# Kernel optimization log

Hardware: AMD Instinct MI355X
Metric: run time of the kernel (lower is better)

The kernel has to match this reference:

```python
import jax, jax.numpy as jnp
import numpy as np

FILTERS = 256
KH, KW = 3, 3
SH, SW = 1, 1
IN_CH = 128


def setup_inputs() -> dict:
    key = jax.random.key(0)
    k1, k2 = jax.random.split(key)
    inputs = jax.random.normal(k1, (32, 112, 112, IN_CH), dtype=jnp.float32)
    # Glorot-uniform init matching the layer's build()
    limit = np.sqrt(6.0 / (KH * KW * IN_CH + FILTERS)).astype(np.float32)
    kernel = jax.random.uniform(k2, (KH, KW, IN_CH, FILTERS), dtype=jnp.float32,
                                minval=-limit, maxval=limit)
    bias = jnp.zeros((FILTERS,), dtype=jnp.float32)
    return {"inputs": inputs, "kernel": kernel, "bias": bias}


def reference(inputs, kernel, bias):
    # Equivalent math to extract_patches(SAME) + flattened matmul + bias:
    # a standard 2D convolution in NHWC with HWIO kernel.
    out = jax.lax.conv_general_dilated(
        inputs, kernel,
        window_strides=(SH, SW),
        padding="SAME",
        dimension_numbers=("NHWC", "HWIO", "NHWC"),
    )
    return out + bias
```

## Files before the change

### kernel.cpp

```cpp
#include <hip/hip_runtime.h>

typedef __attribute__((ext_vector_type(4))) float   floatx4;
typedef __attribute__((ext_vector_type(8))) __bf16  bf16x8;
typedef unsigned short ushort_t;
typedef __attribute__((ext_vector_type(8))) ushort_t ushortx8;

typedef const unsigned int __attribute__((address_space(1)))* gptr_t;
typedef unsigned int __attribute__((address_space(3)))* lptr_t;

#define NIMG 32
#define H    112
#define W    112
#define CIN  128
#define COUT 256
#define HP   114
#define WP   114
#define HW   12544

#define BM 256
#define BN 256
#define BK 64
#define NT 18

#define PREPAD_BLOCKS 12996
#define WTRANS_BLOCKS 1152

__device__ __forceinline__ ushort_t f32_to_bf16(float f) {
    unsigned u = __float_as_uint(f);
    unsigned r = 0x7fffu + ((u >> 16) & 1u);
    return (ushort_t)((u + r) >> 16);
}

__global__ __launch_bounds__(256) void prepass_fused(const float* __restrict__ in,
                                                     const float* __restrict__ k,
                                                     ushort_t* __restrict__ pad,
                                                     ushort_t* __restrict__ wt) {
    int bid = blockIdx.x;
    if (bid < PREPAD_BLOCKS) {
        int u    = bid * 256 + threadIdx.x;
        int ic16 = u & 7;
        int sp   = u >> 3;
        int iw   = sp % WP;
        int sp2  = sp / WP;
        int ih   = sp2 % HP;
        int n    = sp2 / HP;
        ushortx8 v0, v1;
        if (ih >= 1 && ih <= H && iw >= 1 && iw <= W) {
            const float* src = in + ((size_t)((n * H + (ih - 1)) * W + (iw - 1))) * CIN + ic16 * 16;
            floatx4 a = *reinterpret_cast<const floatx4*>(src);
            floatx4 b = *reinterpret_cast<const floatx4*>(src + 4);
            floatx4 c = *reinterpret_cast<const floatx4*>(src + 8);
            floatx4 d = *reinterpret_cast<const floatx4*>(src + 12);
#pragma unroll
            for (int j = 0; j < 4; ++j) {
                v0[j] = f32_to_bf16(a[j]); v0[4 + j] = f32_to_bf16(b[j]);
                v1[j] = f32_to_bf16(c[j]); v1[4 + j] = f32_to_bf16(d[j]);
            }
        } else {
#pragma unroll
            for (int j = 0; j < 8; ++j) { v0[j] = 0; v1[j] = 0; }
        }
        ushortx8* dst = reinterpret_cast<ushortx8*>(pad) + ((size_t)sp * 16 + ic16 * 2);
        dst[0] = v0;
        dst[1] = v1;
    } else {
        int t    = (bid - PREPAD_BLOCKS) * 256 + threadIdx.x;
        int ic   = t & 127;
        int oc   = (t >> 7) & 255;
        int khkw = t >> 15;
        wt[t] = f32_to_bf16(k[((size_t)(khkw * CIN + ic)) * COUT + oc]);
    }
}


__device__ __forceinline__ int aoffK(int t) {
    int tap = t >> 1;
    return ((tap / 3) * WP + (tap % 3)) * CIN + (t & 1) * 64;
}
__device__ __forceinline__ int boffK(int t) {
    int tap = t >> 1;
    return tap * (COUT * CIN) + (t & 1) * 64;
}

__global__ __launch_bounds__(512, 2) void conv_mfma8(const ushort_t* __restrict__ pad,
                                                     const ushort_t* __restrict__ wt,
                                                     const float* __restrict__ bias,
                                                     float* __restrict__ out) {
    __shared__ __align__(16) ushort_t lds[65536];

    const int tid  = threadIdx.x;
    const int wid  = tid >> 6;
    const int lane = tid & 63;
    const int wm   = wid >> 2;
    const int wn   = wid & 3;
    const int bid  = blockIdx.x;
    const int bm   = (bid & 7) * 196 + (bid >> 3);

    const int trow = tid >> 3;
    const int lc   = (tid & 7) ^ (trow & 7);

    const ushort_t* srcA[4];
    const ushort_t* srcB[4];
#pragma unroll
    for (int i = 0; i < 4; ++i) {
        int m  = bm * BM + i * 64 + trow;
        int n  = m / HW;
        int r  = m % HW;
        int oh = r / W;
        int ow = r % W;
        srcA[i] = pad + ((size_t)((n * HP + oh) * WP + ow)) * CIN + lc * 8;
        int oc = i * 64 + trow;
        srcB[i] = wt + (size_t)oc * CIN + lc * 8;
    }
    const int dstSlot = wid * 512;

#define STAGE_A(tile, half)                                                                         \
    { int _o = aoffK(tile); int _b = ((tile) & 1) * 32768 + (half) * 8192 + dstSlot;                \
      __builtin_amdgcn_global_load_lds((gptr_t)(srcA[(half)*2+0] + _o), (lptr_t)&lds[_b       ], 16, 0, 0); \
      __builtin_amdgcn_global_load_lds((gptr_t)(srcA[(half)*2+1] + _o), (lptr_t)&lds[_b + 4096], 16, 0, 0); }
#define STAGE_B(tile, half)                                                                         \
    { int _o = boffK(tile); int _b = ((tile) & 1) * 32768 + 16384 + (half) * 8192 + dstSlot;        \
      __builtin_amdgcn_global_load_lds((gptr_t)(srcB[(half)*2+0] + _o), (lptr_t)&lds[_b       ], 16, 0, 0); \
      __builtin_amdgcn_global_load_lds((gptr_t)(srcB[(half)*2+1] + _o), (lptr_t)&lds[_b + 4096], 16, 0, 0); }

    const int aBase = wm * 8192 + (lane & 15) * 64;
    const int bBase = 16384 + (wn >> 1) * 8192 + ((wn & 1) * 64 + (lane & 15)) * 64;
    int cOff[2];
#pragma unroll
    for (int ks = 0; ks < 2; ++ks)
        cOff[ks] = ((ks * 4 + (lane >> 4)) ^ (lane & 7)) * 8;

    floatx4 acc[8][4];
#pragma unroll
    for (int i = 0; i < 8; ++i)
#pragma unroll
        for (int j = 0; j < 4; ++j) acc[i][j] = (floatx4)0.0f;

    STAGE_A(0, 0); STAGE_A(0, 1); STAGE_B(0, 0); STAGE_B(0, 1);
    STAGE_B(1, 0); STAGE_B(1, 1);
    asm volatile("s_waitcnt vmcnt(4)" ::: "memory");
    __builtin_amdgcn_s_barrier();

    for (int t = 0; t < NT; ++t) {
        const int bufb = (t & 1) * 32768;
        bf16x8 bfr[4][2];
#pragma unroll
        for (int q = 0; q < 4; ++q) {
            bf16x8 af[2][2];
#pragma unroll
            for (int rfl = 0; rfl < 2; ++rfl)
#pragma unroll
                for (int ks = 0; ks < 2; ++ks)
                    af[rfl][ks] = *reinterpret_cast<const bf16x8*>(&lds[bufb + aBase + (2 * q + rfl) * 1024 + cOff[ks]]);
            if (q == 0) {
#pragma unroll
                for (int cf = 0; cf < 2; ++cf)
#pragma unroll
                    for (int ks = 0; ks < 2; ++ks)
                        bfr[cf][ks] = *reinterpret_cast<const bf16x8*>(&lds[bufb + bBase + cf * 1024 + cOff[ks]]);
            }
            if (q == 0 && t + 1 < NT) STAGE_A(t + 1, 0);
            if (q == 1 && t + 1 < NT) STAGE_A(t + 1, 1);
            if (q == 2 && t + 2 < NT) STAGE_B(t + 2, 0);
            if (q == 3 && t + 2 < NT) STAGE_B(t + 2, 1);
            __builtin_amdgcn_s_barrier();
            __builtin_amdgcn_s_setprio(1);
            if (q == 0) {
#pragma unroll
                for (int rfl = 0; rfl < 2; ++rfl)
#pragma unroll
                    for (int cf = 0; cf < 2; ++cf)
#pragma unroll
                        for (int ks = 0; ks < 2; ++ks)
                            acc[rfl][cf] = __builtin_amdgcn_mfma_f32_16x16x32_bf16(
                                af[rfl][ks], bfr[cf][ks], acc[rfl][cf], 0, 0, 0);
#pragma unroll
                for (int cf = 2; cf < 4; ++cf)
#pragma unroll
                    for (int ks = 0; ks < 2; ++ks)
                        bfr[cf][ks] = *reinterpret_cast<const bf16x8*>(&lds[bufb + bBase + cf * 1024 + cOff[ks]]);
#pragma unroll
                for (int rfl = 0; rfl < 2; ++rfl)
#pragma unroll
                    for (int cf = 2; cf < 4; ++cf)
#pragma unroll
                        for (int ks = 0; ks < 2; ++ks)
                            acc[rfl][cf] = __builtin_amdgcn_mfma_f32_16x16x32_bf16(
                                af[rfl][ks], bfr[cf][ks], acc[rfl][cf], 0, 0, 0);
            } else {
#pragma unroll
                for (int rfl = 0; rfl < 2; ++rfl)
#pragma unroll
                    for (int cf = 0; cf < 4; ++cf)
#pragma unroll
                        for (int ks = 0; ks < 2; ++ks)
                            acc[2 * q + rfl][cf] = __builtin_amdgcn_mfma_f32_16x16x32_bf16(
                                af[rfl][ks], bfr[cf][ks], acc[2 * q + rfl][cf], 0, 0, 0);
            }
            __builtin_amdgcn_s_setprio(0);
            if (q == 3) {
                if (t < NT - 2)       { asm volatile("s_waitcnt vmcnt(4)" ::: "memory"); }
                else if (t == NT - 2) { asm volatile("s_waitcnt vmcnt(0)" ::: "memory"); }
            }
            __builtin_amdgcn_s_barrier();
        }
    }

    const int col0 = wn * 64 + (lane & 15);
    const int row0 = bm * BM + wm * 128 + (lane >> 4) * 4;
    float bv[4];
#pragma unroll
    for (int cf = 0; cf < 4; ++cf) bv[cf] = bias[col0 + cf * 16];
#pragma unroll
    for (int rf = 0; rf < 8; ++rf)
#pragma unroll
        for (int cf = 0; cf < 4; ++cf)
#pragma unroll
            for (int r = 0; r < 4; ++r)
                out[(size_t)(row0 + rf * 16 + r) * COUT + col0 + cf * 16] = acc[rf][cf][r] + bv[cf];
#undef STAGE_A
#undef STAGE_B
}

extern "C" void kernel_launch(void* const* d_in, const int* in_sizes, int n_in,
                              void* d_out, int out_size, void* d_ws, size_t ws_size,
                              hipStream_t stream) {
    const float* input = (const float*)d_in[0];
    const float* kern  = (const float*)d_in[1];
    const float* bias  = (const float*)d_in[2];
    float* out         = (float*)d_out;

    ushort_t* pad = (ushort_t*)d_ws;
    ushort_t* wt  = pad + (size_t)NIMG * HP * WP * CIN;

    prepass_fused<<<PREPAD_BLOCKS + WTRANS_BLOCKS, 256, 0, stream>>>(input, kern, pad, wt);
    conv_mfma8<<<1568, 512, 0, stream>>>(pad, wt, bias, out);
}
```

Before: 358.6 us.

## Replace LDS double buffer with single buffer and fine-grained chunk refills

Halves the conv kernel's shared memory from 128KB to 64KB by dropping the double buffer. Each 32-row A chunk and each B half is refilled as soon as the quarter-step that reads it has finished, with per-quarter vmcnt waits. The likely aim is lower LDS footprint, which could let more blocks fit per CU, while keeping loads overlapped with MFMA work. The cost is shorter prefetch distance and tighter waits, so load latency may be exposed more often, and the hand-counted vmcnt values must match exactly to avoid races.

```diff
diff --git a/kernel.cpp b/kernel.cpp
--- a/kernel.cpp
+++ b/kernel.cpp
@@ -72,7 +72,6 @@
     }
 }
 
-
 __device__ __forceinline__ int aoffK(int t) {
     int tap = t >> 1;
     return ((tap / 3) * WP + (tap % 3)) * CIN + (t & 1) * 64;
@@ -81,12 +80,13 @@
     int tap = t >> 1;
     return tap * (COUT * CIN) + (t & 1) * 64;
 }
+
 
 __global__ __launch_bounds__(512, 2) void conv_mfma8(const ushort_t* __restrict__ pad,
                                                      const ushort_t* __restrict__ wt,
                                                      const float* __restrict__ bias,
                                                      float* __restrict__ out) {
-    __shared__ __align__(16) ushort_t lds[65536];
+    __shared__ __align__(16) ushort_t lds[32768];
 
     const int tid  = threadIdx.x;
     const int wid  = tid >> 6;
@@ -96,32 +96,35 @@
     const int bid  = blockIdx.x;
     const int bm   = (bid & 7) * 196 + (bid >> 3);
 
-    const int trow = tid >> 3;
-    const int lc   = (tid & 7) ^ (trow & 7);
-
-    const ushort_t* srcA[4];
-    const ushort_t* srcB[4];
-#pragma unroll
-    for (int i = 0; i < 4; ++i) {
-        int m  = bm * BM + i * 64 + trow;
+    const int rb   = (tid & 255) >> 3;
+    const int half = tid >> 8;
+    const int lc   = (tid & 7) ^ (rb & 7);
+
+    const ushort_t* srcAc[4];
+#pragma unroll
+    for (int q = 0; q < 4; ++q) {
+        int m  = bm * BM + half * 128 + q * 32 + rb;
         int n  = m / HW;
         int r  = m % HW;
         int oh = r / W;
         int ow = r % W;
-        srcA[i] = pad + ((size_t)((n * HP + oh) * WP + ow)) * CIN + lc * 8;
-        int oc = i * 64 + trow;
-        srcB[i] = wt + (size_t)oc * CIN + lc * 8;
-    }
-    const int dstSlot = wid * 512;
-
-#define STAGE_A(tile, half)                                                                         \
-    { int _o = aoffK(tile); int _b = ((tile) & 1) * 32768 + (half) * 8192 + dstSlot;                \
-      __builtin_amdgcn_global_load_lds((gptr_t)(srcA[(half)*2+0] + _o), (lptr_t)&lds[_b       ], 16, 0, 0); \
-      __builtin_amdgcn_global_load_lds((gptr_t)(srcA[(half)*2+1] + _o), (lptr_t)&lds[_b + 4096], 16, 0, 0); }
-#define STAGE_B(tile, half)                                                                         \
-    { int _o = boffK(tile); int _b = ((tile) & 1) * 32768 + 16384 + (half) * 8192 + dstSlot;        \
-      __builtin_amdgcn_global_load_lds((gptr_t)(srcB[(half)*2+0] + _o), (lptr_t)&lds[_b       ], 16, 0, 0); \
-      __builtin_amdgcn_global_load_lds((gptr_t)(srcB[(half)*2+1] + _o), (lptr_t)&lds[_b + 4096], 16, 0, 0); }
+        srcAc[q] = pad + ((size_t)((n * HP + oh) * WP + ow)) * CIN + lc * 8;
+    }
+    const ushort_t* srcB[4];
+#pragma unroll
+    for (int i = 0; i < 4; ++i)
+        srcB[i] = wt + (size_t)(i * 64 + ((tid >> 3) & 63)) * CIN
+                     + (((tid & 7) ^ ((tid >> 3) & 7)) * 8);
+
+    const int awBase   = (wid >> 2) * 8192 + (wid & 3) * 512;
+    const int dstSlotB = wid * 512;
+
+#define STAGE_AC(q_, oA)                                                                            \
+    __builtin_amdgcn_global_load_lds((gptr_t)(srcAc[q_] + (oA)),                                    \
+                                     (lptr_t)&lds[(q_) * 2048 + awBase], 16, 0, 0);
+#define STAGE_B1(j_, oB)                                                                            \
+    __builtin_amdgcn_global_load_lds((gptr_t)(srcB[j_] + (oB)),                                     \
+                                     (lptr_t)&lds[16384 + (j_) * 4096 + dstSlotB], 16, 0, 0);
 
     const int aBase = wm * 8192 + (lane & 15) * 64;
     const int bBase = 16384 + (wn >> 1) * 8192 + ((wn & 1) * 64 + (lane & 15)) * 64;
@@ -136,13 +139,19 @@
 #pragma unroll
         for (int j = 0; j < 4; ++j) acc[i][j] = (floatx4)0.0f;
 
-    STAGE_A(0, 0); STAGE_A(0, 1); STAGE_B(0, 0); STAGE_B(0, 1);
-    STAGE_B(1, 0); STAGE_B(1, 1);
-    asm volatile("s_waitcnt vmcnt(4)" ::: "memory");
+    {
+        const int oA0 = aoffK(0);
+        const int oB0 = boffK(0);
+        STAGE_AC(0, oA0); STAGE_AC(1, oA0); STAGE_AC(2, oA0);
+        STAGE_B1(0, oB0); STAGE_B1(1, oB0); STAGE_B1(2, oB0); STAGE_B1(3, oB0);
+    }
+    asm volatile("s_waitcnt vmcnt(0)" ::: "memory");
     __builtin_amdgcn_s_barrier();
 
     for (int t = 0; t < NT; ++t) {
-        const int bufb = (t & 1) * 32768;
+        const int oAc = aoffK(t);
+        const int oAn = aoffK(t + 1);
+        const int oBn = boffK(t + 1);
         bf16x8 bfr[4][2];
 #pragma unroll
         for (int q = 0; q < 4; ++q) {
@@ -151,18 +160,18 @@
             for (int rfl = 0; rfl < 2; ++rfl)
 #pragma unroll
                 for (int ks = 0; ks < 2; ++ks)
-                    af[rfl][ks] = *reinterpret_cast<const bf16x8*>(&lds[bufb + aBase + (2 * q + rfl) * 1024 + cOff[ks]]);
+                    af[rfl][ks] = *reinterpret_cast<const bf16x8*>(&lds[aBase + (2 * q + rfl) * 1024 + cOff[ks]]);
             if (q == 0) {
 #pragma unroll
                 for (int cf = 0; cf < 2; ++cf)
 #pragma unroll
                     for (int ks = 0; ks < 2; ++ks)
-                        bfr[cf][ks] = *reinterpret_cast<const bf16x8*>(&lds[bufb + bBase + cf * 1024 + cOff[ks]]);
-            }
-            if (q == 0 && t + 1 < NT) STAGE_A(t + 1, 0);
-            if (q == 1 && t + 1 < NT) STAGE_A(t + 1, 1);
-            if (q == 2 && t + 2 < NT) STAGE_B(t + 2, 0);
-            if (q == 3 && t + 2 < NT) STAGE_B(t + 2, 1);
+                        bfr[cf][ks] = *reinterpret_cast<const bf16x8*>(&lds[bBase + cf * 1024 + cOff[ks]]);
+            }
+            if (q == 0) { STAGE_AC(3, oAc); }
+            if (q == 1 && t + 1 < NT) { STAGE_AC(0, oAn); STAGE_B1(0, oBn); STAGE_B1(1, oBn); }
+            if (q == 2 && t + 1 < NT) { STAGE_AC(1, oAn); STAGE_B1(2, oBn); STAGE_B1(3, oBn); }
+            if (q == 3 && t + 1 < NT) { STAGE_AC(2, oAn); }
             __builtin_amdgcn_s_barrier();
             __builtin_amdgcn_s_setprio(1);
             if (q == 0) {
@@ -178,7 +187,7 @@
                 for (int cf = 2; cf < 4; ++cf)
 #pragma unroll
                     for (int ks = 0; ks < 2; ++ks)
-                        bfr[cf][ks] = *reinterpret_cast<const bf16x8*>(&lds[bufb + bBase + cf * 1024 + cOff[ks]]);
+                        bfr[cf][ks] = *reinterpret_cast<const bf16x8*>(&lds[bBase + cf * 1024 + cOff[ks]]);
 #pragma unroll
                 for (int rfl = 0; rfl < 2; ++rfl)
 #pragma unroll
@@ -198,10 +207,15 @@
                                 af[rfl][ks], bfr[cf][ks], acc[2 * q + rfl][cf], 0, 0, 0);
             }
             __builtin_amdgcn_s_setprio(0);
-            if (q == 3) {
-                if (t < NT - 2)       { asm volatile("s_waitcnt vmcnt(4)" ::: "memory"); }
-                else if (t == NT - 2) { asm volatile("s_waitcnt vmcnt(0)" ::: "memory"); }
-            }
+            if (q == 1) {
+                if (t < NT - 1) { asm volatile("s_waitcnt vmcnt(4)" ::: "memory"); }
+                else            { asm volatile("s_waitcnt vmcnt(1)" ::: "memory"); }
+            }
+            if (q == 2) {
+                if (t < NT - 1) { asm volatile("s_waitcnt vmcnt(6)" ::: "memory"); }
+                else            { asm volatile("s_waitcnt vmcnt(0)" ::: "memory"); }
+            }
+            if (q == 3) { asm volatile("s_waitcnt vmcnt(1)" ::: "memory"); }
             __builtin_amdgcn_s_barrier();
         }
     }
@@ -218,8 +232,8 @@
 #pragma unroll
             for (int r = 0; r < 4; ++r)
                 out[(size_t)(row0 + rf * 16 + r) * COUT + col0 + cf * 16] = acc[rf][cf][r] + bv[cf];
-#undef STAGE_A
-#undef STAGE_B
+#undef STAGE_AC
+#undef STAGE_B1
 }
 
 extern "C" void kernel_launch(void* const* d_in, const int* in_sizes, int n_in,
```

After: 352.6 us. About the same (-1.7%).
